# Kernel tuning notes

Measured on AMD Instinct MI355X. Metric: run time of the kernel, lower is better.

Reference implementation:

```python
import jax, jax.numpy as jnp
import numpy as np
import math

HIDDEN = 1024
NUM_HEADS = 16
NUM_GROUPS = 16  # source einsum/rearrange only shape-checks when groups == heads
HEAD_DIM = HIDDEN // NUM_HEADS


def rope(x, base=10000.0):
    # x: [b, s, d]; applied to the FULL hidden vector before head split, as in source.
    # Source rope_fn has a reshape bug; this is the intended rotate-half RoPE with
    # half_d frequencies 1/base^(i/half_d) (== 1/base^(2i/d)).
    b, s, d = x.shape
    half = d // 2
    x1, x2 = x[..., :half], x[..., half:]
    pos = jnp.arange(s, dtype=x.dtype)[:, None]                          # [s,1]
    inv_freq = 1.0 / (base ** (jnp.arange(half, dtype=x.dtype) / half))  # [half]
    ang = pos * inv_freq[None, :]                                        # [s,half]
    sin = jnp.sin(ang)[None]                                             # [1,s,half]
    cos = jnp.cos(ang)[None]
    return jnp.concatenate([x1 * cos - x2 * sin, x2 * cos + x1 * sin], axis=-1)


def setup_inputs() -> dict:
    key = jax.random.key(0)
    ks = jax.random.split(key, 10)
    scale = 1.0 / math.sqrt(HIDDEN)
    inp = {
        "x": jax.random.normal(ks[0], (2, 2048, HIDDEN), dtype=jnp.float32),
        "attn_mask": jax.random.randint(ks[1], (2, 2048), 0, 2, dtype=jnp.int32),
        "Wq": jax.random.uniform(ks[2], (HIDDEN, HIDDEN), jnp.float32, -scale, scale),
        "bq": jax.random.uniform(ks[3], (HIDDEN,), jnp.float32, -scale, scale),
        "Wk": jax.random.uniform(ks[4], (HIDDEN, HIDDEN), jnp.float32, -scale, scale),
        "bk": jax.random.uniform(ks[5], (HIDDEN,), jnp.float32, -scale, scale),
        "Wv": jax.random.uniform(ks[6], (HIDDEN, HIDDEN), jnp.float32, -scale, scale),
        "bv": jax.random.uniform(ks[7], (HIDDEN,), jnp.float32, -scale, scale),
        "Wo": jax.random.uniform(ks[8], (HIDDEN, HIDDEN), jnp.float32, -scale, scale),
        "bo": jax.random.uniform(ks[9], (HIDDEN,), jnp.float32, -scale, scale),
    }
    return inp


def reference(x, attn_mask, Wq, bq, Wk, bk, Wv, bv, Wo, bo):
    b, s, _ = x.shape
    g = NUM_GROUPS
    subh = NUM_HEADS // g  # = 1 here
    d = HIDDEN // g        # per-group dim (== head dim when g == h)

    q = rope(x @ Wq.T + bq)
    k = rope(x @ Wk.T + bk)
    v = x @ Wv.T + bv

    # q: b s (g subh d) -> b g subh s d ; k,v: b s (g d) -> b g s d
    q = q.reshape(b, s, g, subh, d).transpose(0, 2, 3, 1, 4)
    k = k.reshape(b, s, g, d).transpose(0, 2, 1, 3)
    v = v.reshape(b, s, g, d).transpose(0, 2, 1, 3)

    e = jnp.einsum('bghqd,bgkd->bghqk', q, k) / math.sqrt(HEAD_DIM)  # [b,g,subh,s,s]
    mask5 = attn_mask[:, None, None, None, :]  # broadcast over g, subh, query
    e = jnp.where(mask5 == 0, -jnp.inf, e)
    attn = jax.nn.softmax(e, axis=-1)
    out = jnp.einsum('bghqk,bgkd->bghqd', attn, v)            # [b,g,subh,s,d]
    out = out.transpose(0, 3, 1, 2, 4).reshape(b, s, HIDDEN)  # b s (g subh d)
    return out @ Wo.T + bo
```

## Files before the change

kernel.cpp:

```cpp
#include <hip/hip_runtime.h>
#include <hip/hip_bf16.h>


constexpr int Bb  = 2;
constexpr int Ss  = 2048;
constexpr int Hh  = 1024;
constexpr int NHh = 16;
constexpr int Mm  = Bb * Ss;

typedef __attribute__((ext_vector_type(8))) unsigned short ushort8;
typedef __attribute__((ext_vector_type(8))) short short8;
typedef __attribute__((ext_vector_type(4))) float f32x4;
typedef __attribute__((ext_vector_type(4))) unsigned int u32x4;

__device__ __forceinline__ unsigned short f2bf(float f) {
    unsigned int u = __float_as_uint(f);
    u += 0x7fffu + ((u >> 16) & 1u);
    return (unsigned short)(u >> 16);
}
__device__ __forceinline__ float bf2f(unsigned short h) {
    return __uint_as_float(((unsigned int)h) << 16);
}
__device__ __forceinline__ void gload16(const void* g, void* l) {
    __builtin_amdgcn_global_load_lds(
        (const __attribute__((address_space(1))) unsigned int*)g,
        (__attribute__((address_space(3))) unsigned int*)l, 16, 0, 0);
}

__global__ __launch_bounds__(256) void convert_k(
    const float* __restrict__ x,
    const float* __restrict__ Wq, const float* __restrict__ Wk,
    const float* __restrict__ Wv, const float* __restrict__ Wo,
    unsigned short* __restrict__ xb, unsigned short* __restrict__ wall)
{
    size_t e = ((size_t)blockIdx.x * 256 + threadIdx.x) << 3;
    const float* s; unsigned short* d;
    if (e < (size_t)Mm * Hh) {
        s = x + e; d = xb + e;
    } else {
        size_t f = e - (size_t)Mm * Hh;
        int t = (int)(f >> 20);
        const float* w = (t == 0) ? Wq : (t == 1) ? Wk : (t == 2) ? Wv : Wo;
        s = w + (f & 1048575);
        d = wall + f;
    }
    float4 a = *(const float4*)s;
    float4 b = *(const float4*)(s + 4);
    ushort8 o;
    o[0] = f2bf(a.x); o[1] = f2bf(a.y); o[2] = f2bf(a.z); o[3] = f2bf(a.w);
    o[4] = f2bf(b.x); o[5] = f2bf(b.y); o[6] = f2bf(b.z); o[7] = f2bf(b.w);
    *(ushort8*)d = o;
}

__global__ __launch_bounds__(256) void maskbf_k(
    const int* __restrict__ am, unsigned short* __restrict__ maskbf)
{
    int i = blockIdx.x * 256 + threadIdx.x;
    maskbf[i] = am[i] ? (unsigned short)0x3F80 : (unsigned short)0;
}

#define GEMM_BODY(ATYPE_PTR, WPTR, K0MAX)                                          \
    __shared__ unsigned short As[128 * 64];                                        \
    __shared__ unsigned short Bs[128 * 64];                                        \
    const int tid  = threadIdx.x;                                                  \
    const int lane = tid & 63;                                                     \
    const int w    = tid >> 6;                                                     \
    const int wr   = w >> 1, wc = w & 1;                                           \
    const int l16  = lane & 15, g = lane >> 4;                                     \
    const int R0   = blockIdx.x * 128;                                             \
    char* asb = (char*)As; char* bsb = (char*)Bs;                                  \
    f32x4 acc[4][4] = {};                                                          \
    for (int k0 = 0; k0 < K0MAX; k0 += 64) {                                       \
        _Pragma("unroll")                                                          \
        for (int it = 0; it < 4; ++it) {                                           \
            int sbase = w * 4096 + it * 1024;                                      \
            int boff  = sbase + lane * 16;                                         \
            int r     = boff >> 7;                                                 \
            int c     = (boff >> 4) & 7;                                           \
            int col   = k0 + ((c ^ (r & 7)) << 3);                                 \
            gload16(&ATYPE_PTR[(size_t)(R0 + r) * 1024 + col], asb + sbase);       \
            gload16(&WPTR[(size_t)(gn + r) * 1024 + col], bsb + sbase);            \
        }                                                                          \
        __syncthreads();                                                           \
        short8 bfrag[4][2];                                                        \
        _Pragma("unroll")                                                          \
        for (int u = 0; u < 4; ++u) {                                              \
            int row = wc * 64 + u * 16 + l16;                                      \
            _Pragma("unroll")                                                      \
            for (int s = 0; s < 2; ++s)                                            \
                bfrag[u][s] = *(const short8*)(bsb + row * 128 +                   \
                               ((s * 64 + g * 16) ^ ((row & 7) << 4)));            \
        }                                                                          \
        _Pragma("unroll")                                                          \
        for (int t = 0; t < 4; ++t) {                                              \
            int row = wr * 64 + t * 16 + l16;                                      \
            short8 af[2];                                                          \
            _Pragma("unroll")                                                      \
            for (int s = 0; s < 2; ++s)                                            \
                af[s] = *(const short8*)(asb + row * 128 +                         \
                         ((s * 64 + g * 16) ^ ((row & 7) << 4)));                  \
            _Pragma("unroll")                                                      \
            for (int u = 0; u < 4; ++u) {                                          \
                acc[t][u] = __builtin_amdgcn_mfma_f32_16x16x32_bf16(af[0], bfrag[u][0], acc[t][u], 0, 0, 0); \
                acc[t][u] = __builtin_amdgcn_mfma_f32_16x16x32_bf16(af[1], bfrag[u][1], acc[t][u], 0, 0, 0); \
            }                                                                      \
        }                                                                          \
        __syncthreads();                                                           \
    }

__global__ __launch_bounds__(256) void gemm_qkv_k(
    const unsigned short* __restrict__ xb, const unsigned short* __restrict__ wall,
    const float* __restrict__ bq, const float* __restrict__ bk, const float* __restrict__ bv,
    unsigned short* __restrict__ q, unsigned short* __restrict__ k2,
    unsigned short* __restrict__ v)
{
    const int gn = blockIdx.y * 128;
    GEMM_BODY(xb, wall, 1024)

    const int sel = gn >> 10;
    const int n0  = gn & 1023;
    const float* bias = (sel == 0) ? bq : (sel == 1) ? bk : bv;
    unsigned short* outp = (sel == 0) ? q : (sel == 1) ? k2 : v;
    const float qs = (sel == 0) ? 0.18033688011112042f : 1.0f;
    #pragma unroll
    for (int u = 0; u < 4; ++u) {
        int coll = wc * 64 + u * 16 + l16;
        float bb = bias[n0 + coll];
        #pragma unroll
        for (int t = 0; t < 4; ++t)
            #pragma unroll
            for (int rr = 0; rr < 4; ++rr) {
                int row = R0 + wr * 64 + t * 16 + g * 4 + rr;
                outp[(size_t)row * 1024 + n0 + coll] = f2bf((acc[t][u][rr] + bb) * qs);
            }
    }
}

__global__ __launch_bounds__(256) void gemm_out_k(
    const unsigned short* __restrict__ ao, const unsigned short* __restrict__ wo,
    const float* __restrict__ bo, float* __restrict__ out)
{
    const int gn = blockIdx.y * 128;
    GEMM_BODY(ao, wo, 1024)

    #pragma unroll
    for (int u = 0; u < 4; ++u) {
        int coll = wc * 64 + u * 16 + l16;
        float bb = bo[gn + coll];
        #pragma unroll
        for (int t = 0; t < 4; ++t)
            #pragma unroll
            for (int rr = 0; rr < 4; ++rr) {
                int row = R0 + wr * 64 + t * 16 + g * 4 + rr;
                out[(size_t)row * 1024 + gn + coll] = acc[t][u][rr] + bb;
            }
    }
}

__global__ __launch_bounds__(256) void rope_frag_k(
    const unsigned short* __restrict__ qin, const unsigned short* __restrict__ kin,
    unsigned short* __restrict__ qfrag, unsigned short* __restrict__ kfrag)
{
    __shared__ unsigned short Ld[2][64][72];
    const int kt = blockIdx.x;
    const int hp = blockIdx.y;
    const int zz = blockIdx.z;
    const int bz = zz & 1, sel = zz >> 1;
    const unsigned short* src = sel ? kin : qin;
    unsigned short* dstf = sel ? kfrag : qfrag;

    const int t   = threadIdx.x;
    const int r   = t & 63;
    const int c16 = (t >> 6) << 4;
    const int pos = kt * 64 + r;
    const size_t rowb = (size_t)(bz * Ss + pos) * 1024;

    ushort8 A0 = *(const ushort8*)&src[rowb + hp * 64 + c16];
    ushort8 A1 = *(const ushort8*)&src[rowb + hp * 64 + c16 + 8];
    ushort8 B0 = *(const ushort8*)&src[rowb + (hp + 8) * 64 + c16];
    ushort8 B1 = *(const ushort8*)&src[rowb + (hp + 8) * 64 + c16 + 8];

    #pragma unroll
    for (int i = 0; i < 16; ++i) {
        int d = c16 + i;
        float jj  = (float)(hp * 64 + d);
        float inv = exp2f(jj * -0.0259525632621414f);
        float ang = (float)pos * inv;
        float sn, cs;
        __sincosf(ang, &sn, &cs);
        unsigned short ua = (i < 8) ? A0[i] : A1[i - 8];
        unsigned short ub = (i < 8) ? B0[i] : B1[i - 8];
        float a = bf2f(ua), b = bf2f(ub);
        Ld[0][r][d] = f2bf(a * cs - b * sn);
        Ld[1][r][d] = f2bf(b * cs + a * sn);
    }
    __syncthreads();

    #pragma unroll
    for (int cc = 0; cc < 4; ++cc) {
        int c    = t * 4 + cc;
        int hh   = c >> 9;
        int ci   = c & 511;
        int blk  = ci >> 7, s2 = (ci >> 6) & 1, lane2 = ci & 63;
        int gg = lane2 >> 4, ll = lane2 & 15;
        ushort8 o = *(const ushort8*)&Ld[hh][blk * 16 + ll][s2 * 32 + gg * 8];
        size_t base = (size_t)(bz * 16 + hp + hh * 8) * 131072 + (size_t)kt * 4096;
        *(ushort8*)&dstf[base + (size_t)ci * 8] = o;
    }
}

__global__ __launch_bounds__(256) void fragify_v_k(
    const unsigned short* __restrict__ v, const int* __restrict__ mask,
    unsigned short* __restrict__ vfrag)
{
    __shared__ unsigned short Ld[64][72];
    __shared__ int Lm[64];
    const int kt = blockIdx.x, bh = blockIdx.y;
    const int bz = bh >> 4, h = bh & 15;
    const int t = threadIdx.x;
    const int r = t & 63, c0 = (t >> 6) << 4;
    const unsigned short* srcp = &v[(size_t)(bz * Ss + kt * 64 + r) * 1024 + h * 64 + c0];
    *(ushort8*)&Ld[r][c0]     = *(const ushort8*)srcp;
    *(ushort8*)&Ld[r][c0 + 8] = *(const ushort8*)(srcp + 8);
    if (t < 64) Lm[t] = mask[bz * Ss + kt * 64 + t];
    __syncthreads();

    #pragma unroll
    for (int cc = 0; cc < 2; ++cc) {
        int c = t * 2 + cc;
        int dt4 = c >> 7, ks = (c >> 6) & 1, lane2 = c & 63;
        int gg = lane2 >> 4, ll = lane2 & 15;
        ushort8 o;
        #pragma unroll
        for (int e = 0; e < 8; ++e) {
            int key = ks * 32 + gg * 8 + e;
            o[e] = Lm[key] ? Ld[key][dt4 * 16 + ll] : (unsigned short)0;
        }
        *(ushort8*)&vfrag[(size_t)bh * 131072 + (size_t)kt * 4096 + (size_t)c * 8] = o;
    }
}

#define FLASH_ITER(KC, KN, KT)                                                     \
    {                                                                              \
        const int ktn = kt0 + ((((KT) - kt0) + 1) & 15);                           \
        _Pragma("unroll")                                                          \
        for (int i = 0; i < 8; ++i)                                                \
            KN[i] = *(const short8*)&kfb[(size_t)ktn * 4096 + i * 512 + lane * 8]; \
        _Pragma("unroll")                                                          \
        for (int i = 0; i < 8; ++i)                                                \
            VV[i] = *(const short8*)&vfb[(size_t)(KT) * 4096 + i * 512 + lane * 8];\
        short8 mf[2];                                                              \
        mf[0] = *(const short8*)&mbz[(KT) * 64 + g * 8];                           \
        mf[1] = *(const short8*)&mbz[(KT) * 64 + 32 + g * 8];                      \
        f32x4 S[2][4];                                                             \
        _Pragma("unroll")                                                          \
        for (int t = 0; t < 2; ++t)                                                \
            _Pragma("unroll")                                                      \
            for (int k4 = 0; k4 < 4; ++k4) S[t][k4] = (f32x4)0.f;                  \
        _Pragma("unroll")                                                          \
        for (int k4 = 0; k4 < 4; ++k4)                                             \
            _Pragma("unroll")                                                      \
            for (int t = 0; t < 2; ++t) {                                          \
                S[t][k4] = __builtin_amdgcn_mfma_f32_16x16x32_bf16(                \
                    KC[k4 * 2 + 0], qf[t][0], S[t][k4], 0, 0, 0);                  \
                S[t][k4] = __builtin_amdgcn_mfma_f32_16x16x32_bf16(                \
                    KC[k4 * 2 + 1], qf[t][1], S[t][k4], 0, 0, 0);                  \
            }                                                                      \
        float rm[2];                                                               \
        _Pragma("unroll")                                                          \
        for (int t = 0; t < 2; ++t) {                                              \
            float m0 = fmaxf(fmaxf(S[t][0][0], S[t][0][1]), fmaxf(S[t][0][2], S[t][0][3])); \
            float m1 = fmaxf(fmaxf(S[t][1][0], S[t][1][1]), fmaxf(S[t][1][2], S[t][1][3])); \
            float m2 = fmaxf(fmaxf(S[t][2][0], S[t][2][1]), fmaxf(S[t][2][2], S[t][2][3])); \
            float m3 = fmaxf(fmaxf(S[t][3][0], S[t][3][1]), fmaxf(S[t][3][2], S[t][3][3])); \
            float m  = fmaxf(fmaxf(m0, m1), fmaxf(m2, m3));                        \
            m = fmaxf(m, __shfl_xor(m, 16));                                       \
            m = fmaxf(m, __shfl_xor(m, 32));                                       \
            rm[t] = m;                                                             \
        }                                                                          \
        bool grow = (rm[0] > mrow[0] + 10.0f) || (rm[1] > mrow[1] + 10.0f);        \
        if (__any((int)grow)) {                                                    \
            float mn0 = fmaxf(mrow[0], rm[0]);                                     \
            float mn1 = fmaxf(mrow[1], rm[1]);                                     \
            float rs0 = exp2f(mrow[0] - mn0);                                      \
            float rs1 = exp2f(mrow[1] - mn1);                                      \
            mrow[0] = mn0; mrow[1] = mn1;                                          \
            _Pragma("unroll")                                                      \
            for (int r = 0; r < 4; ++r) {                                          \
                float f0 = __shfl(rs0, g * 4 + r);                                 \
                float f1 = __shfl(rs1, g * 4 + r);                                 \
                _Pragma("unroll")                                                  \
                for (int dt = 0; dt < 4; ++dt) { O[0][dt][r] *= f0; O[1][dt][r] *= f1; } \
                Osum[0][r] *= f0; Osum[1][r] *= f1;                                \
            }                                                                      \
        }                                                                          \
        _Pragma("unroll")                                                          \
        for (int t = 0; t < 2; ++t) {                                              \
            unsigned int U[4][2];                                                  \
            _Pragma("unroll")                                                      \
            for (int k4 = 0; k4 < 4; ++k4) {                                       \
                float p0 = exp2f(S[t][k4][0] - mrow[t]);                           \
                float p1 = exp2f(S[t][k4][1] - mrow[t]);                           \
                float p2 = exp2f(S[t][k4][2] - mrow[t]);                           \
                float p3 = exp2f(S[t][k4][3] - mrow[t]);                           \
                asm("v_cvt_pk_bf16_f32 %0, %1, %2" : "=v"(U[k4][0]) : "v"(p0), "v"(p1)); \
                asm("v_cvt_pk_bf16_f32 %0, %1, %2" : "=v"(U[k4][1]) : "v"(p2), "v"(p3)); \
            }                                                                      \
            asm("v_permlane32_swap_b32 %0, %1" : "+v"(U[0][0]), "+v"(U[1][0]));    \
            asm("v_permlane32_swap_b32 %0, %1" : "+v"(U[0][1]), "+v"(U[1][1]));    \
            asm("v_permlane32_swap_b32 %0, %1" : "+v"(U[2][0]), "+v"(U[3][0]));    \
            asm("v_permlane32_swap_b32 %0, %1" : "+v"(U[2][1]), "+v"(U[3][1]));    \
            asm("v_permlane16_swap_b32 %0, %1" : "+v"(U[0][0]), "+v"(U[1][0]));    \
            asm("v_permlane16_swap_b32 %0, %1" : "+v"(U[0][1]), "+v"(U[1][1]));    \
            asm("v_permlane16_swap_b32 %0, %1" : "+v"(U[2][0]), "+v"(U[3][0]));    \
            asm("v_permlane16_swap_b32 %0, %1" : "+v"(U[2][1]), "+v"(U[3][1]));    \
            _Pragma("unroll")                                                      \
            for (int ks = 0; ks < 2; ++ks) {                                       \
                u32x4 gp;                                                          \
                gp[0] = U[2 * ks][0]; gp[1] = U[2 * ks][1];                        \
                gp[2] = U[2 * ks + 1][0]; gp[3] = U[2 * ks + 1][1];                \
                short8 pf = __builtin_bit_cast(short8, gp);                        \
                Osum[t] = __builtin_amdgcn_mfma_f32_16x16x32_bf16(pf, mf[ks], Osum[t], 0, 0, 0); \
                _Pragma("unroll")                                                  \
                for (int dt = 0; dt < 4; ++dt)                                     \
                    O[t][dt] = __builtin_amdgcn_mfma_f32_16x16x32_bf16(            \
                        pf, VV[dt * 2 + ks], O[t][dt], 0, 0, 0);                   \
            }                                                                      \
        }                                                                          \
    }

__global__ __launch_bounds__(256, 2) void flash_k(
    const unsigned short* __restrict__ qfrag, const unsigned short* __restrict__ kfrag,
    const unsigned short* __restrict__ vfrag, const unsigned short* __restrict__ maskbf,
    unsigned short* __restrict__ opart, float2* __restrict__ ml)
{
    const int F   = blockIdx.x;
    const int xcd = F & 7, j = F >> 3;
    const int grp = xcd * 4 + (j >> 5);
    const int rem = j & 31;
    const int qb  = rem >> 1;
    const int half = rem & 1;
    const int h   = grp & 15;
    const int bz  = grp >> 4;
    const int kt0 = half * 16;

    const int tid  = threadIdx.x;
    const int lane = tid & 63;
    const int w    = tid >> 6;
    const int l16  = lane & 15;
    const int g    = lane >> 4;

    const size_t fb = (size_t)(bz * 16 + h) * 131072;
    const unsigned short* kfb = kfrag + fb;
    const unsigned short* vfb = vfrag + fb;
    const unsigned short* qfb = qfrag + fb;
    const unsigned short* mbz = maskbf + bz * Ss;

    short8 qf[2][2];
    #pragma unroll
    for (int t = 0; t < 2; ++t)
        #pragma unroll
        for (int s = 0; s < 2; ++s)
            qf[t][s] = *(const short8*)&qfb[(size_t)(qb * 8 + w * 2 + t) * 1024
                                            + s * 512 + lane * 8];

    f32x4 O[2][4];
    #pragma unroll
    for (int t = 0; t < 2; ++t)
        #pragma unroll
        for (int d = 0; d < 4; ++d) O[t][d] = (f32x4)0.f;
    f32x4 Osum[2];
    Osum[0] = (f32x4)0.f; Osum[1] = (f32x4)0.f;
    float mrow[2] = {-1.0e4f, -1.0e4f};

    short8 KA[8], KB[8], VV[8];
    #pragma unroll
    for (int i = 0; i < 8; ++i)
        KA[i] = *(const short8*)&kfb[(size_t)kt0 * 4096 + i * 512 + lane * 8];

    for (int kt2 = 0; kt2 < 16; kt2 += 2) {
        FLASH_ITER(KA, KB, kt0 + kt2)
        FLASH_ITER(KB, KA, kt0 + kt2 + 1)
    }

    const size_t NE = (size_t)Mm * Hh;
    #pragma unroll
    for (int t = 0; t < 2; ++t)
        #pragma unroll
        for (int r = 0; r < 4; ++r) {
            float osum = Osum[t][r];
            float inv  = osum > 0.f ? 1.0f / osum : 0.f;
            float mo   = __shfl(mrow[t], g * 4 + r);
            int rowl   = qb * 128 + w * 32 + t * 16 + g * 4 + r;
            size_t ob  = (size_t)half * NE
                       + ((size_t)(bz * Ss + rowl)) * 1024 + h * 64;
            #pragma unroll
            for (int dt = 0; dt < 4; ++dt)
                opart[ob + dt * 16 + l16] = f2bf(O[t][dt][r] * inv);
            if (l16 == 0)
                ml[((half * 2 + bz) * 16 + h) * 2048 + rowl] = make_float2(mo, osum);
        }
}

__global__ __launch_bounds__(256) void combine_k(
    const unsigned short* __restrict__ opart, const float2* __restrict__ ml,
    unsigned short* __restrict__ ao)
{
    const size_t NE = (size_t)Mm * Hh;
    int c    = blockIdx.x * 256 + threadIdx.x;
    int row  = c >> 7;
    int col8 = c & 127;
    int h    = col8 >> 3;
    int bz   = row >> 11, qrow = row & 2047;

    float2 a = ml[((0 * 2 + bz) * 16 + h) * 2048 + qrow];
    float2 b = ml[((1 * 2 + bz) * 16 + h) * 2048 + qrow];
    float M  = fmaxf(a.x, b.x);
    float w1 = exp2f(a.x - M) * a.y;
    float w2 = exp2f(b.x - M) * b.y;
    float tot = w1 + w2;
    float inv = tot > 0.f ? 1.0f / tot : 0.f;
    w1 *= inv; w2 *= inv;

    ushort8 o1 = *(const ushort8*)&opart[(size_t)c * 8];
    ushort8 o2 = *(const ushort8*)&opart[NE + (size_t)c * 8];
    ushort8 o;
    #pragma unroll
    for (int jj = 0; jj < 8; ++jj)
        o[jj] = f2bf(bf2f(o1[jj]) * w1 + bf2f(o2[jj]) * w2);
    *(ushort8*)&ao[(size_t)c * 8] = o;
}

extern "C" void kernel_launch(void* const* d_in, const int* in_sizes, int n_in,
                              void* d_out, int out_size, void* d_ws, size_t ws_size,
                              hipStream_t stream)
{
    const float* x  = (const float*)d_in[0];
    const int*   am = (const int*)d_in[1];
    const float* Wq = (const float*)d_in[2];
    const float* bq = (const float*)d_in[3];
    const float* Wk = (const float*)d_in[4];
    const float* bk = (const float*)d_in[5];
    const float* Wv = (const float*)d_in[6];
    const float* bv = (const float*)d_in[7];
    const float* Wo = (const float*)d_in[8];
    const float* bo = (const float*)d_in[9];
    float* out = (float*)d_out;

    const size_t NE = (size_t)Mm * Hh;
    unsigned short* q     = (unsigned short*)d_ws;
    unsigned short* k     = q + NE;
    unsigned short* v     = k + NE;
    unsigned short* ao    = v + NE;
    unsigned short* xb    = ao + NE;
    unsigned short* wall  = xb + NE;
    unsigned short* wo    = wall + 3u * 1048576u;
    unsigned short* kfrag = wall + 4u * 1048576u;
    unsigned short* qfrag = xb;
    unsigned short* vfrag = q;
    unsigned short* opart = k;
    float2*         ml    = (float2*)(kfrag + 4u * 1048576u);
    unsigned short* maskbf = (unsigned short*)(ml + 131072);

    convert_k<<<(2 * NE) / (256 * 8), 256, 0, stream>>>(x, Wq, Wk, Wv, Wo, xb, wall);
    maskbf_k<<<dim3(Mm / 256), 256, 0, stream>>>(am, maskbf);
    gemm_qkv_k<<<dim3(Mm / 128, 3072 / 128), 256, 0, stream>>>(
        xb, wall, bq, bk, bv, q, k, v);
    rope_frag_k<<<dim3(32, 8, 4), 256, 0, stream>>>(q, k, qfrag, kfrag);
    fragify_v_k<<<dim3(32, 32), 256, 0, stream>>>(v, am, vfrag);
    flash_k<<<dim3(1024), 256, 0, stream>>>(qfrag, kfrag, vfrag, maskbf, opart, ml);
    combine_k<<<dim3((Mm * 128) / 256), 256, 0, stream>>>(opart, ml, ao);
    gemm_out_k<<<dim3(Mm / 128, Hh / 128), 256, 0, stream>>>(ao, wo, bo, out);
}
```

Measured before the change: 162.1 us.

## Shrink flash attention per-wave tile to one 16-row Q block for occupancy

Each wave in the flash kernel now handles a single 16-row query tile instead of two. Block q-size drops from 128 to 64 rows, so the grid doubles to 2048 blocks and launch bounds rise to 4 blocks per CU. The K double-buffer prefetch is dropped in favour of a simple per-iteration load, and V is loaded in two halves to lower register pressure. The aim is higher occupancy to hide latency, at the cost of K/V fragments being reloaded twice as often per query row and losing explicit prefetch.

Result: slower. 175.0 us (+8.0%).

```diff
diff --git a/kernel.cpp b/kernel.cpp
--- a/kernel.cpp
+++ b/kernel.cpp
@@ -240,109 +240,20 @@
     }
 }
 
-#define FLASH_ITER(KC, KN, KT)                                                     \
-    {                                                                              \
-        const int ktn = kt0 + ((((KT) - kt0) + 1) & 15);                           \
-        _Pragma("unroll")                                                          \
-        for (int i = 0; i < 8; ++i)                                                \
-            KN[i] = *(const short8*)&kfb[(size_t)ktn * 4096 + i * 512 + lane * 8]; \
-        _Pragma("unroll")                                                          \
-        for (int i = 0; i < 8; ++i)                                                \
-            VV[i] = *(const short8*)&vfb[(size_t)(KT) * 4096 + i * 512 + lane * 8];\
-        short8 mf[2];                                                              \
-        mf[0] = *(const short8*)&mbz[(KT) * 64 + g * 8];                           \
-        mf[1] = *(const short8*)&mbz[(KT) * 64 + 32 + g * 8];                      \
-        f32x4 S[2][4];                                                             \
-        _Pragma("unroll")                                                          \
-        for (int t = 0; t < 2; ++t)                                                \
-            _Pragma("unroll")                                                      \
-            for (int k4 = 0; k4 < 4; ++k4) S[t][k4] = (f32x4)0.f;                  \
-        _Pragma("unroll")                                                          \
-        for (int k4 = 0; k4 < 4; ++k4)                                             \
-            _Pragma("unroll")                                                      \
-            for (int t = 0; t < 2; ++t) {                                          \
-                S[t][k4] = __builtin_amdgcn_mfma_f32_16x16x32_bf16(                \
-                    KC[k4 * 2 + 0], qf[t][0], S[t][k4], 0, 0, 0);                  \
-                S[t][k4] = __builtin_amdgcn_mfma_f32_16x16x32_bf16(                \
-                    KC[k4 * 2 + 1], qf[t][1], S[t][k4], 0, 0, 0);                  \
-            }                                                                      \
-        float rm[2];                                                               \
-        _Pragma("unroll")                                                          \
-        for (int t = 0; t < 2; ++t) {                                              \
-            float m0 = fmaxf(fmaxf(S[t][0][0], S[t][0][1]), fmaxf(S[t][0][2], S[t][0][3])); \
-            float m1 = fmaxf(fmaxf(S[t][1][0], S[t][1][1]), fmaxf(S[t][1][2], S[t][1][3])); \
-            float m2 = fmaxf(fmaxf(S[t][2][0], S[t][2][1]), fmaxf(S[t][2][2], S[t][2][3])); \
-            float m3 = fmaxf(fmaxf(S[t][3][0], S[t][3][1]), fmaxf(S[t][3][2], S[t][3][3])); \
-            float m  = fmaxf(fmaxf(m0, m1), fmaxf(m2, m3));                        \
-            m = fmaxf(m, __shfl_xor(m, 16));                                       \
-            m = fmaxf(m, __shfl_xor(m, 32));                                       \
-            rm[t] = m;                                                             \
-        }                                                                          \
-        bool grow = (rm[0] > mrow[0] + 10.0f) || (rm[1] > mrow[1] + 10.0f);        \
-        if (__any((int)grow)) {                                                    \
-            float mn0 = fmaxf(mrow[0], rm[0]);                                     \
-            float mn1 = fmaxf(mrow[1], rm[1]);                                     \
-            float rs0 = exp2f(mrow[0] - mn0);                                      \
-            float rs1 = exp2f(mrow[1] - mn1);                                      \
-            mrow[0] = mn0; mrow[1] = mn1;                                          \
-            _Pragma("unroll")                                                      \
-            for (int r = 0; r < 4; ++r) {                                          \
-                float f0 = __shfl(rs0, g * 4 + r);                                 \
-                float f1 = __shfl(rs1, g * 4 + r);                                 \
-                _Pragma("unroll")                                                  \
-                for (int dt = 0; dt < 4; ++dt) { O[0][dt][r] *= f0; O[1][dt][r] *= f1; } \
-                Osum[0][r] *= f0; Osum[1][r] *= f1;                                \
-            }                                                                      \
-        }                                                                          \
-        _Pragma("unroll")                                                          \
-        for (int t = 0; t < 2; ++t) {                                              \
-            unsigned int U[4][2];                                                  \
-            _Pragma("unroll")                                                      \
-            for (int k4 = 0; k4 < 4; ++k4) {                                       \
-                float p0 = exp2f(S[t][k4][0] - mrow[t]);                           \
-                float p1 = exp2f(S[t][k4][1] - mrow[t]);                           \
-                float p2 = exp2f(S[t][k4][2] - mrow[t]);                           \
-                float p3 = exp2f(S[t][k4][3] - mrow[t]);                           \
-                asm("v_cvt_pk_bf16_f32 %0, %1, %2" : "=v"(U[k4][0]) : "v"(p0), "v"(p1)); \
-                asm("v_cvt_pk_bf16_f32 %0, %1, %2" : "=v"(U[k4][1]) : "v"(p2), "v"(p3)); \
-            }                                                                      \
-            asm("v_permlane32_swap_b32 %0, %1" : "+v"(U[0][0]), "+v"(U[1][0]));    \
-            asm("v_permlane32_swap_b32 %0, %1" : "+v"(U[0][1]), "+v"(U[1][1]));    \
-            asm("v_permlane32_swap_b32 %0, %1" : "+v"(U[2][0]), "+v"(U[3][0]));    \
-            asm("v_permlane32_swap_b32 %0, %1" : "+v"(U[2][1]), "+v"(U[3][1]));    \
-            asm("v_permlane16_swap_b32 %0, %1" : "+v"(U[0][0]), "+v"(U[1][0]));    \
-            asm("v_permlane16_swap_b32 %0, %1" : "+v"(U[0][1]), "+v"(U[1][1]));    \
-            asm("v_permlane16_swap_b32 %0, %1" : "+v"(U[2][0]), "+v"(U[3][0]));    \
-            asm("v_permlane16_swap_b32 %0, %1" : "+v"(U[2][1]), "+v"(U[3][1]));    \
-            _Pragma("unroll")                                                      \
-            for (int ks = 0; ks < 2; ++ks) {                                       \
-                u32x4 gp;                                                          \
-                gp[0] = U[2 * ks][0]; gp[1] = U[2 * ks][1];                        \
-                gp[2] = U[2 * ks + 1][0]; gp[3] = U[2 * ks + 1][1];                \
-                short8 pf = __builtin_bit_cast(short8, gp);                        \
-                Osum[t] = __builtin_amdgcn_mfma_f32_16x16x32_bf16(pf, mf[ks], Osum[t], 0, 0, 0); \
-                _Pragma("unroll")                                                  \
-                for (int dt = 0; dt < 4; ++dt)                                     \
-                    O[t][dt] = __builtin_amdgcn_mfma_f32_16x16x32_bf16(            \
-                        pf, VV[dt * 2 + ks], O[t][dt], 0, 0, 0);                   \
-            }                                                                      \
-        }                                                                          \
-    }
-
-__global__ __launch_bounds__(256, 2) void flash_k(
+__global__ __launch_bounds__(256, 4) void flash_k(
     const unsigned short* __restrict__ qfrag, const unsigned short* __restrict__ kfrag,
     const unsigned short* __restrict__ vfrag, const unsigned short* __restrict__ maskbf,
     unsigned short* __restrict__ opart, float2* __restrict__ ml)
 {
-    const int F   = blockIdx.x;
-    const int xcd = F & 7, j = F >> 3;
-    const int grp = xcd * 4 + (j >> 5);
-    const int rem = j & 31;
-    const int qb  = rem >> 1;
+    const int F    = blockIdx.x;
+    const int xcd  = F & 7, j = F >> 3;
+    const int grp  = xcd * 4 + (j >> 6);
+    const int rem  = j & 63;
+    const int qb   = rem >> 1;
     const int half = rem & 1;
-    const int h   = grp & 15;
-    const int bz  = grp >> 4;
-    const int kt0 = half * 16;
+    const int h    = grp & 15;
+    const int bz   = grp >> 4;
+    const int kt0  = half * 16;
 
     const int tid  = threadIdx.x;
     const int lane = tid & 63;
@@ -356,50 +267,112 @@
     const unsigned short* qfb = qfrag + fb;
     const unsigned short* mbz = maskbf + bz * Ss;
 
-    short8 qf[2][2];
-    #pragma unroll
-    for (int t = 0; t < 2; ++t)
-        #pragma unroll
-        for (int s = 0; s < 2; ++s)
-            qf[t][s] = *(const short8*)&qfb[(size_t)(qb * 8 + w * 2 + t) * 1024
-                                            + s * 512 + lane * 8];
-
-    f32x4 O[2][4];
-    #pragma unroll
-    for (int t = 0; t < 2; ++t)
-        #pragma unroll
-        for (int d = 0; d < 4; ++d) O[t][d] = (f32x4)0.f;
-    f32x4 Osum[2];
-    Osum[0] = (f32x4)0.f; Osum[1] = (f32x4)0.f;
-    float mrow[2] = {-1.0e4f, -1.0e4f};
-
-    short8 KA[8], KB[8], VV[8];
-    #pragma unroll
-    for (int i = 0; i < 8; ++i)
-        KA[i] = *(const short8*)&kfb[(size_t)kt0 * 4096 + i * 512 + lane * 8];
-
-    for (int kt2 = 0; kt2 < 16; kt2 += 2) {
-        FLASH_ITER(KA, KB, kt0 + kt2)
-        FLASH_ITER(KB, KA, kt0 + kt2 + 1)
+    short8 qf0 = *(const short8*)&qfb[(size_t)(qb * 4 + w) * 1024 + lane * 8];
+    short8 qf1 = *(const short8*)&qfb[(size_t)(qb * 4 + w) * 1024 + 512 + lane * 8];
+
+    f32x4 O[4];
+    #pragma unroll
+    for (int d = 0; d < 4; ++d) O[d] = (f32x4)0.f;
+    f32x4 Osum = (f32x4)0.f;
+    float mrow = -1.0e4f;
+
+    for (int kt = kt0; kt < kt0 + 16; ++kt) {
+        short8 KC[8];
+        #pragma unroll
+        for (int i = 0; i < 8; ++i)
+            KC[i] = *(const short8*)&kfb[(size_t)kt * 4096 + i * 512 + lane * 8];
+        short8 mf0 = *(const short8*)&mbz[kt * 64 + g * 8];
+        short8 mf1 = *(const short8*)&mbz[kt * 64 + 32 + g * 8];
+
+        f32x4 S[4];
+        #pragma unroll
+        for (int k4 = 0; k4 < 4; ++k4) S[k4] = (f32x4)0.f;
+        #pragma unroll
+        for (int k4 = 0; k4 < 4; ++k4) {
+            S[k4] = __builtin_amdgcn_mfma_f32_16x16x32_bf16(KC[k4 * 2 + 0], qf0, S[k4], 0, 0, 0);
+            S[k4] = __builtin_amdgcn_mfma_f32_16x16x32_bf16(KC[k4 * 2 + 1], qf1, S[k4], 0, 0, 0);
+        }
+
+        short8 V0[4];
+        #pragma unroll
+        for (int dt = 0; dt < 4; ++dt)
+            V0[dt] = *(const short8*)&vfb[(size_t)kt * 4096 + (dt * 2) * 512 + lane * 8];
+
+        float m0 = fmaxf(fmaxf(S[0][0], S[0][1]), fmaxf(S[0][2], S[0][3]));
+        float m1 = fmaxf(fmaxf(S[1][0], S[1][1]), fmaxf(S[1][2], S[1][3]));
+        float m2 = fmaxf(fmaxf(S[2][0], S[2][1]), fmaxf(S[2][2], S[2][3]));
+        float m3 = fmaxf(fmaxf(S[3][0], S[3][1]), fmaxf(S[3][2], S[3][3]));
+        float m  = fmaxf(fmaxf(m0, m1), fmaxf(m2, m3));
+        m = fmaxf(m, __shfl_xor(m, 16));
+        m = fmaxf(m, __shfl_xor(m, 32));
+
+        if (__any((int)(m > mrow + 10.0f))) {
+            float mn = fmaxf(mrow, m);
+            float rs = exp2f(mrow - mn);
+            mrow = mn;
+            #pragma unroll
+            for (int r = 0; r < 4; ++r) {
+                float f0 = __shfl(rs, g * 4 + r);
+                #pragma unroll
+                for (int dt = 0; dt < 4; ++dt) O[dt][r] *= f0;
+                Osum[r] *= f0;
+            }
+        }
+
+        unsigned int U[4][2];
+        #pragma unroll
+        for (int k4 = 0; k4 < 4; ++k4) {
+            float p0 = exp2f(S[k4][0] - mrow);
+            float p1 = exp2f(S[k4][1] - mrow);
+            float p2 = exp2f(S[k4][2] - mrow);
+            float p3 = exp2f(S[k4][3] - mrow);
+            asm("v_cvt_pk_bf16_f32 %0, %1, %2" : "=v"(U[k4][0]) : "v"(p0), "v"(p1));
+            asm("v_cvt_pk_bf16_f32 %0, %1, %2" : "=v"(U[k4][1]) : "v"(p2), "v"(p3));
+        }
+        asm("v_permlane32_swap_b32 %0, %1" : "+v"(U[0][0]), "+v"(U[1][0]));
+        asm("v_permlane32_swap_b32 %0, %1" : "+v"(U[0][1]), "+v"(U[1][1]));
+        asm("v_permlane32_swap_b32 %0, %1" : "+v"(U[2][0]), "+v"(U[3][0]));
+        asm("v_permlane32_swap_b32 %0, %1" : "+v"(U[2][1]), "+v"(U[3][1]));
+        asm("v_permlane16_swap_b32 %0, %1" : "+v"(U[0][0]), "+v"(U[1][0]));
+        asm("v_permlane16_swap_b32 %0, %1" : "+v"(U[0][1]), "+v"(U[1][1]));
+        asm("v_permlane16_swap_b32 %0, %1" : "+v"(U[2][0]), "+v"(U[3][0]));
+        asm("v_permlane16_swap_b32 %0, %1" : "+v"(U[2][1]), "+v"(U[3][1]));
+
+        u32x4 gp0, gp1;
+        gp0[0] = U[0][0]; gp0[1] = U[0][1]; gp0[2] = U[1][0]; gp0[3] = U[1][1];
+        gp1[0] = U[2][0]; gp1[1] = U[2][1]; gp1[2] = U[3][0]; gp1[3] = U[3][1];
+        short8 pf0 = __builtin_bit_cast(short8, gp0);
+        short8 pf1 = __builtin_bit_cast(short8, gp1);
+
+        Osum = __builtin_amdgcn_mfma_f32_16x16x32_bf16(pf0, mf0, Osum, 0, 0, 0);
+        #pragma unroll
+        for (int dt = 0; dt < 4; ++dt)
+            O[dt] = __builtin_amdgcn_mfma_f32_16x16x32_bf16(pf0, V0[dt], O[dt], 0, 0, 0);
+
+        short8 V1[4];
+        #pragma unroll
+        for (int dt = 0; dt < 4; ++dt)
+            V1[dt] = *(const short8*)&vfb[(size_t)kt * 4096 + (dt * 2 + 1) * 512 + lane * 8];
+        Osum = __builtin_amdgcn_mfma_f32_16x16x32_bf16(pf1, mf1, Osum, 0, 0, 0);
+        #pragma unroll
+        for (int dt = 0; dt < 4; ++dt)
+            O[dt] = __builtin_amdgcn_mfma_f32_16x16x32_bf16(pf1, V1[dt], O[dt], 0, 0, 0);
     }
 
     const size_t NE = (size_t)Mm * Hh;
     #pragma unroll
-    for (int t = 0; t < 2; ++t)
-        #pragma unroll
-        for (int r = 0; r < 4; ++r) {
-            float osum = Osum[t][r];
-            float inv  = osum > 0.f ? 1.0f / osum : 0.f;
-            float mo   = __shfl(mrow[t], g * 4 + r);
-            int rowl   = qb * 128 + w * 32 + t * 16 + g * 4 + r;
-            size_t ob  = (size_t)half * NE
-                       + ((size_t)(bz * Ss + rowl)) * 1024 + h * 64;
-            #pragma unroll
-            for (int dt = 0; dt < 4; ++dt)
-                opart[ob + dt * 16 + l16] = f2bf(O[t][dt][r] * inv);
-            if (l16 == 0)
-                ml[((half * 2 + bz) * 16 + h) * 2048 + rowl] = make_float2(mo, osum);
-        }
+    for (int r = 0; r < 4; ++r) {
+        float osum = Osum[r];
+        float inv  = osum > 0.f ? 1.0f / osum : 0.f;
+        float mo   = __shfl(mrow, g * 4 + r);
+        int rowl   = qb * 64 + w * 16 + g * 4 + r;
+        size_t ob  = (size_t)half * NE + ((size_t)(bz * Ss + rowl)) * 1024 + h * 64;
+        #pragma unroll
+        for (int dt = 0; dt < 4; ++dt)
+            opart[ob + dt * 16 + l16] = f2bf(O[dt][r] * inv);
+        if (l16 == 0)
+            ml[((half * 2 + bz) * 16 + h) * 2048 + rowl] = make_float2(mo, osum);
+    }
 }
 
 __global__ __launch_bounds__(256) void combine_k(
@@ -468,7 +441,7 @@
         xb, wall, bq, bk, bv, q, k, v);
     rope_frag_k<<<dim3(32, 8, 4), 256, 0, stream>>>(q, k, qfrag, kfrag);
     fragify_v_k<<<dim3(32, 32), 256, 0, stream>>>(v, am, vfrag);
-    flash_k<<<dim3(1024), 256, 0, stream>>>(qfrag, kfrag, vfrag, maskbf, opart, ml);
+    flash_k<<<dim3(2048), 256, 0, stream>>>(qfrag, kfrag, vfrag, maskbf, opart, ml);
     combine_k<<<dim3((Mm * 128) / 256), 256, 0, stream>>>(opart, ml, ao);
     gemm_out_k<<<dim3(Mm / 128, Hh / 128), 256, 0, stream>>>(ao, wo, bo, out);
 }
```
